# Kernel tuning notes

Hardware: AMD Instinct MI355X
Metric: run time of the kernel (lower is better)

The kernel has to match this reference:

```python
import jax, jax.numpy as jnp
import numpy as np

B, NQ, L, E, K = 64, 1024, 128, 8192, 2
LN_EPS = 1e-5


def setup_inputs() -> dict:
    key = jax.random.key(0)
    ks = jax.random.split(key, 16)
    s1 = 1.0 / np.sqrt(2 * L + 1)
    s2 = 1.0 / np.sqrt(L)
    s3 = 1.0 / np.sqrt(2 * L)
    return {
        "z0": jax.random.normal(ks[0], (B, L), jnp.float32),
        "edge_index": jax.random.randint(ks[1], (2, E), 0, NQ, jnp.int64),
        "edge_attr": jax.random.normal(ks[2], (E,), jnp.float32),
        "n_qubits": NQ,
        # edge MLP params, stacked over K message-passing rounds
        "e_w1": jax.random.normal(ks[3], (K, L, 2 * L + 1), jnp.float32) * s1,
        "e_b1": jnp.zeros((K, L), jnp.float32),
        "e_w2": jax.random.normal(ks[4], (K, L, L), jnp.float32) * s2,
        "e_b2": jnp.zeros((K, L), jnp.float32),
        # node MLP params
        "n_w1": jax.random.normal(ks[5], (K, L, 2 * L), jnp.float32) * s3,
        "n_b1": jnp.zeros((K, L), jnp.float32),
        "ln_g": jnp.ones((K, L), jnp.float32),
        "ln_b": jnp.zeros((K, L), jnp.float32),
        "n_w2": jax.random.normal(ks[6], (K, L, L), jnp.float32) * s2,
        "n_b2": jnp.zeros((K, L), jnp.float32),
    }


def reference(z0, edge_index, edge_attr, n_qubits,
              e_w1, e_b1, e_w2, e_b2,
              n_w1, n_b1, ln_g, ln_b, n_w2, n_b2):
    b, l = z0.shape
    src, tgt = edge_index[0], edge_index[1]
    e_ = src.shape[0]
    # broadcast latent z0 to every node: h [B, N, L]
    h = jnp.broadcast_to(z0[:, None, :], (b, n_qubits, l))
    e = jnp.broadcast_to(edge_attr[None, :, None], (b, e_, 1))  # [B, E, 1]
    k_rounds = e_w1.shape[0]
    for k in range(k_rounds):
        hi = h[:, src, :]  # gather source node feats [B, E, L]
        hj = h[:, tgt, :]  # gather target node feats [B, E, L]
        inp_e = jnp.concatenate([hi, hj, e], axis=-1)  # [B, E, 2L+1]
        m = jax.nn.relu(inp_e @ e_w1[k].T + e_b1[k]) @ e_w2[k].T + e_b2[k]
        # scatter_add messages back to source nodes
        m_agg = jnp.zeros_like(h).at[:, src, :].add(m)
        inp_n = jnp.concatenate([h, m_agg], axis=-1)  # [B, N, 2L]
        x = jax.nn.relu(inp_n @ n_w1[k].T + n_b1[k])
        mu = x.mean(axis=-1, keepdims=True)
        var = ((x - mu) ** 2).mean(axis=-1, keepdims=True)
        x = (x - mu) * jax.lax.rsqrt(var + LN_EPS) * ln_g[k] + ln_b[k]
        # Dropout(p=0.1) is identity in eval mode
        h = x @ n_w2[k].T + n_b2[k] + h  # residual
    return h.mean(axis=1)  # [B, L]
```

## Files before the change

### kernel.cpp

```cpp
#include <hip/hip_runtime.h>

#define B_   64
#define NQ_  1024
#define L_   128
#define E_   8192
#define M_   (B_*NQ_)
#define LDP  136
#define TILE 2176

typedef unsigned short u16;
typedef unsigned int   u32;
typedef unsigned long long u64;
typedef __attribute__((ext_vector_type(8))) short short8;
typedef __attribute__((ext_vector_type(4))) float floatx4;

#define WVB() __builtin_amdgcn_wave_barrier()

__device__ __forceinline__ int imax2(int a, int b) { return a > b ? a : b; }

__device__ __forceinline__ u16 f2bf(float f) {
    union { float f; u32 u; } v; v.f = f;
    return (u16)((v.u + 0x7fffu + ((v.u >> 16) & 1u)) >> 16);
}
__device__ __forceinline__ float bf2f(u16 u) {
    union { u32 u; float f; } v; v.u = ((u32)u) << 16;
    return v.f;
}
__device__ __forceinline__ floatx4 mfma16(short8 a, short8 b, floatx4 c) {
    return __builtin_amdgcn_mfma_f32_16x16x32_bf16(a, b, c, 0, 0, 0);
}
__device__ __forceinline__ short8 sfrag(const u16* t, int r0, int kb, int lane) {
    return *(const short8*)(t + (r0 + (lane & 15)) * LDP + kb * 32 + (lane >> 4) * 8);
}
__device__ __forceinline__ short8 wfrag(const u16* wf, int nt, int kb, int lane) {
    return *(const short8*)(wf + (((kb << 3) + nt) * 64 + lane) * 8);
}
__device__ __forceinline__ void frag_flush(const u16* t, u16* wf, int nt, int lane) {
#pragma unroll
    for (int kb = 0; kb < 4; ++kb)
        *(short8*)(wf + (((kb << 3) + nt) * 64 + lane) * 8) = sfrag(t, 0, kb, lane);
}
__device__ __forceinline__ short8 frag_cvt(const float* base, int r0, int ld, int kb, int lane) {
    const float* p = base + (size_t)(r0 + (lane & 15)) * ld + kb * 32 + (lane >> 4) * 8;
    short8 s;
#pragma unroll
    for (int j = 0; j < 8; ++j) s[j] = (short)f2bf(p[j]);
    return s;
}
__device__ __forceinline__ void tile_store(u16* t, const floatx4* acc, int lane) {
    int col = lane & 15, qd = lane >> 4;
#pragma unroll
    for (int nt = 0; nt < 8; ++nt)
#pragma unroll
        for (int r = 0; r < 4; ++r)
            t[(qd * 4 + r) * LDP + nt * 16 + col] = f2bf(acc[nt][r]);
}
__device__ __forceinline__ void tile_flush(const u16* t, u16* g, int lane) {
#pragma unroll
    for (int it = 0; it < 4; ++it) {
        int chunk = it * 64 + lane, row = chunk >> 4, c8 = chunk & 15;
        *(uint4*)(g + (size_t)row * 128 + c8 * 8) = *(const uint4*)(t + row * LDP + c8 * 8);
    }
}
__device__ __forceinline__ int blk_swz() {
    int r = blockIdx.x;
    int b = (((r >> 3) & 7) << 3) | (r & 7);
    return b * 16 + (r >> 6);
}

struct P {
    const int* ei; const float* attr; const float* z0;
    const float* e_w1; const float* e_b1; const float* e_w2; const float* e_b2;
    const float* n_w1; const float* n_b1; const float* ln_g; const float* ln_b;
    const float* n_w2; const float* n_b2;
    int* ofs; int* tgt_s; float* a_s; float* degf;
    u16* wf;
    u16* w_n20;
    float* wl; float* vb2;
    float* rx; float* rci; float* rcj; float* rh; float* mx0;
    u16* c0t; u16* t1g; u16* ci1; u16* cj1;
    float* out;
};

__global__ __launch_bounds__(256) void k_setup(P p) {
    __shared__ __align__(16) char smem[17408];
    int tid = threadIdx.x, blk = blockIdx.x;
    int lane = tid & 63, w = tid >> 6, col = lane & 15, qd = lane >> 4;

    if (blk == 0) {
        __shared__ int cnt[1024];
        __shared__ int wsum[4];
        __shared__ int flag;
#pragma unroll
        for (int i = 0; i < 4; ++i) cnt[tid + i * 256] = 0;
        if (tid == 0) flag = 1;
        __syncthreads();
        if (tid < 100 && p.ei[2 * tid + 1] != 0) atomicAnd(&flag, 0);
        __syncthreads();
        int i64 = flag;
        for (int e = tid; e < E_; e += 256) {
            int s = i64 ? p.ei[2 * e] : p.ei[e];
            atomicAdd(&cnt[s], 1);
        }
        __syncthreads();
        int q0 = tid * 4;
        int c0 = cnt[q0], c1 = cnt[q0 + 1], c2 = cnt[q0 + 2], c3 = cnt[q0 + 3];
        int tsum = c0 + c1 + c2 + c3, incl = tsum;
#pragma unroll
        for (int o = 1; o < 64; o <<= 1) {
            int t = __shfl_up(incl, o, 64);
            if (lane >= o) incl += t;
        }
        if (lane == 63) wsum[w] = incl;
        __syncthreads();
        int wo = 0;
        for (int i = 0; i < w; ++i) wo += wsum[i];
        int base = wo + incl - tsum;
        p.ofs[q0] = base; p.ofs[q0 + 1] = base + c0;
        p.ofs[q0 + 2] = base + c0 + c1; p.ofs[q0 + 3] = base + c0 + c1 + c2;
        p.degf[q0] = (float)c0; p.degf[q0 + 1] = (float)c1;
        p.degf[q0 + 2] = (float)c2; p.degf[q0 + 3] = (float)c3;
        if (tid == 0) p.ofs[NQ_] = E_;
        __syncthreads();
        cnt[q0] = base; cnt[q0 + 1] = base + c0;
        cnt[q0 + 2] = base + c0 + c1; cnt[q0 + 3] = base + c0 + c1 + c2;
        __syncthreads();
        for (int e = tid; e < E_; e += 256) {
            int s = i64 ? p.ei[2 * e]        : p.ei[e];
            int t = i64 ? p.ei[2 * (E_ + e)] : p.ei[E_ + e];
            int pos = atomicAdd(&cnt[s], 1);
            p.tgt_s[pos] = t;
            p.a_s[pos]   = p.attr[e];
        }
    } else if (blk <= 2) {
        int base = (blk - 1) * 8192;
        for (int idx = tid; idx < 8192; idx += 256)
            p.w_n20[base + idx] = f2bf(p.n_w2[base + idx]);
    } else if (blk == 3) {
        const float* src = p.n_w2 + 16384;
        u16* dst = p.wf + 5 * 16384;
        for (int pr = w; pr < 32; pr += 4) {
            int kb = pr >> 3, nt = pr & 7;
            const float* s = src + (nt * 16 + col) * 128 + kb * 32 + qd * 8;
            short8 v;
#pragma unroll
            for (int j = 0; j < 8; ++j) v[j] = (short)f2bf(s[j]);
            *(short8*)(dst + (pr * 64 + lane) * 8) = v;
        }
    } else if (blk <= 13) {
        int g = (blk - 4) >> 1, part = (blk - 4) & 1;
        const float* Pm; const float* Q; int ldp; u16* D;
        switch (g) {
            case 0:  Pm = p.n_w1 + 128;             ldp = 256; Q = p.e_w2;         D = p.wf;             break;
            case 1:  Pm = p.n_w1 + 32768 + 128;     ldp = 256; Q = p.e_w2 + 16384; D = p.wf + 4 * 16384; break;
            case 2:  Pm = p.e_w1 + 128 * 257;       ldp = 257; Q = p.n_w2;         D = p.wf + 1 * 16384; break;
            case 3:  Pm = p.e_w1 + 128 * 257 + 128; ldp = 257; Q = p.n_w2;         D = p.wf + 2 * 16384; break;
            default: Pm = p.n_w1 + 32768;           ldp = 256; Q = p.n_w2;         D = p.wf + 3 * 16384; break;
        }
        int tile = part * 4 + w;
        int r0 = tile * 16;
        floatx4 acc[8] = {};
#pragma unroll
        for (int kb = 0; kb < 4; ++kb) {
            short8 a = frag_cvt(Pm, r0, ldp, kb, lane);
#pragma unroll
            for (int nt = 0; nt < 8; ++nt) {
                short8 bq;
#pragma unroll
                for (int j = 0; j < 8; ++j)
                    bq[j] = (short)f2bf(Q[(kb * 32 + qd * 8 + j) * 128 + nt * 16 + col]);
                acc[nt] = mfma16(a, bq, acc[nt]);
            }
        }
        u16* slot = (u16*)smem + w * TILE;
        tile_store(slot, acc, lane); WVB();
        frag_flush(slot, D, tile, lane);
    } else if (blk == 14) {
        int r0 = w * 16;
        floatx4 acc[8] = {};
#pragma unroll
        for (int kb = 0; kb < 4; ++kb) {
            short8 a = frag_cvt(p.z0, r0, 128, kb, lane);
#pragma unroll
            for (int nt = 0; nt < 8; ++nt)
                acc[nt] = mfma16(a, frag_cvt(p.n_w1, nt * 16, 256, kb, lane), acc[nt]);
        }
#pragma unroll
        for (int nt = 0; nt < 8; ++nt) {
            int cg = nt * 16 + col; float bv = p.n_b1[cg];
#pragma unroll
            for (int r = 0; r < 4; ++r) p.rx[(r0 + qd * 4 + r) * 128 + cg] = acc[nt][r] + bv;
        }
    } else if (blk <= 17) {
        int r0 = w * 16;
        const float* Wp; int ld; const float* bias; float* dst;
        if (blk == 15)      { Wp = p.e_w1 + 128 * 257;       ld = 257; bias = p.e_b1 + 128; dst = p.rci; }
        else if (blk == 16) { Wp = p.e_w1 + 128 * 257 + 128; ld = 257; bias = nullptr;      dst = p.rcj; }
        else                { Wp = p.n_w1 + 32768;           ld = 256; bias = p.n_b1 + 128; dst = p.rh;  }
        floatx4 acc[8] = {};
#pragma unroll
        for (int kb = 0; kb < 4; ++kb) {
            short8 a;
            int rr = (r0 + col) * 128, kk = kb * 32 + qd * 8;
#pragma unroll
            for (int j = 0; j < 8; ++j) a[j] = (short)f2bf(p.z0[rr + kk + j] + p.n_b2[kk + j]);
#pragma unroll
            for (int nt = 0; nt < 8; ++nt)
                acc[nt] = mfma16(a, frag_cvt(Wp, nt * 16, ld, kb, lane), acc[nt]);
        }
#pragma unroll
        for (int nt = 0; nt < 8; ++nt) {
            int cg = nt * 16 + col;
            float bv = bias ? bias[cg] : 0.0f;
#pragma unroll
            for (int r = 0; r < 4; ++r) dst[(r0 + qd * 4 + r) * 128 + cg] = acc[nt][r] + bv;
        }
    } else if (blk == 18) {
        int r0 = w * 16;
        floatx4 a1[8] = {};
#pragma unroll
        for (int kb = 0; kb < 4; ++kb) {
            short8 a = frag_cvt(p.z0, r0, 128, kb, lane);
#pragma unroll
            for (int nt = 0; nt < 8; ++nt) {
                a1[nt] = mfma16(a, frag_cvt(p.e_w1,       nt * 16, 257, kb, lane), a1[nt]);
                a1[nt] = mfma16(a, frag_cvt(p.e_w1 + 128, nt * 16, 257, kb, lane), a1[nt]);
            }
        }
#pragma unroll
        for (int nt = 0; nt < 8; ++nt) {
            float bv = p.e_b1[nt * 16 + col];
#pragma unroll
            for (int r = 0; r < 4; ++r) a1[nt][r] += bv;
        }
        u16* slot = (u16*)smem + w * TILE;
        tile_store(slot, a1, lane); WVB();
        tile_flush(slot, p.c0t + (size_t)r0 * 128, lane);
    } else {
        int k = tid >> 7, c = tid & 127;
        const float4* wp = (const float4*)(p.n_w1 + k * 32768 + c * 256 + 128);
        const float4* bp = (const float4*)(p.e_b2 + k * 128);
        float s0 = 0.f, s1 = 0.f, s2 = 0.f, s3 = 0.f;
#pragma unroll
        for (int n4 = 0; n4 < 32; ++n4) {
            float4 a = wp[n4], bv = bp[n4];
            s0 += a.x * bv.x; s1 += a.y * bv.y; s2 += a.z * bv.z; s3 += a.w * bv.w;
        }
        p.vb2[tid] = (s0 + s1) + (s2 + s3);
        p.wl[tid]  = p.e_w1[k * 128 * 257 + c * 257 + 256];
        for (int i = tid; i < 8192; i += 256) p.mx0[i] = 0.0f;
    }
}

__global__ __launch_bounds__(256, 4) void k_node0(P p) {
    __shared__ __align__(16) char smem[34816];
    u16* xt = (u16*)smem;
    u16* ob = (u16*)(smem + 17408);
    int tid = threadIdx.x, lane = tid & 63, w = tid >> 6;
    int col = lane & 15, qd = lane >> 4;
    int blk = blk_swz();
    int rowbase = blk * 64 + w * 16;
    int b = blk >> 4;

    {
        u32 cv = ((const u32*)p.c0t)[b * 64 + lane];
        float cx = bf2f((u16)(cv & 0xffffu)), cy = bf2f((u16)(cv >> 16));
        float2 wl2 = ((const float2*)p.wl)[lane];
        for (int qq = 0; qq < 16; qq += 4) {
            int st[4], en[4];
            float ax[4] = {}, ay[4] = {};
#pragma unroll
            for (int j = 0; j < 4; ++j) {
                int q = (rowbase + qq + j) & (NQ_ - 1);
                st[j] = p.ofs[q]; en[j] = p.ofs[q + 1];
            }
            int mx = imax2(imax2(en[0] - st[0], en[1] - st[1]),
                           imax2(en[2] - st[2], en[3] - st[3]));
            for (int k2 = 0; k2 < mx; ++k2) {
#pragma unroll
                for (int j = 0; j < 4; ++j) {
                    int idx = st[j] + k2, last = en[j] - 1;
                    int safe = idx < en[j] ? idx : (last >= 0 ? last : 0);
                    float a = p.a_s[safe];
                    float vx = fmaxf(cx + a * wl2.x, 0.f);
                    float vy = fmaxf(cy + a * wl2.y, 0.f);
                    bool v = idx < en[j];
                    ax[j] += v ? vx : 0.f;
                    ay[j] += v ? vy : 0.f;
                }
            }
#pragma unroll
            for (int j = 0; j < 4; ++j) {
                int r = qq + j;
                u32* tp = (u32*)(xt + (size_t)w * TILE + r * LDP);
                tp[lane] = (u32)f2bf(ax[j]) | ((u32)f2bf(ay[j]) << 16);
            }
        }
    }
    WVB();

    floatx4 xa[8] = {};
#pragma unroll
    for (int kb = 0; kb < 4; ++kb) {
        short8 a = sfrag(xt + w * TILE, 0, kb, lane);
#pragma unroll
        for (int nt = 0; nt < 8; ++nt) xa[nt] = mfma16(a, wfrag(p.wf, nt, kb, lane), xa[nt]);
    }
    WVB();
    float s8[8] = {};
#pragma unroll
    for (int nt = 0; nt < 8; ++nt) {
        int cg = nt * 16 + col;
        float base = p.rx[b * 128 + cg], vb = p.vb2[cg];
#pragma unroll
        for (int r = 0; r < 4; ++r) {
            int row = rowbase + qd * 4 + r;
            xa[nt][r] = fmaxf(xa[nt][r] + base + p.degf[row & (NQ_ - 1)] * vb, 0.f);
        }
    }
#pragma unroll
    for (int r = 0; r < 4; ++r) {
        float s = 0.f, s2 = 0.f;
#pragma unroll
        for (int nt = 0; nt < 8; ++nt) { float v = xa[nt][r]; s += v; s2 += v * v; }
#pragma unroll
        for (int o = 1; o < 16; o <<= 1) { s += __shfl_xor(s, o, 64); s2 += __shfl_xor(s2, o, 64); }
        float mu = s * (1.f / 128.f), var = s2 * (1.f / 128.f) - mu * mu;
        float rs = rsqrtf(var + 1e-5f);
#pragma unroll
        for (int nt = 0; nt < 8; ++nt) {
            int cg = nt * 16 + col;
            float xv = (xa[nt][r] - mu) * rs * p.ln_g[cg] + p.ln_b[cg];
            xa[nt][r] = xv;
            s8[nt] += xv;
        }
    }
    tile_store(xt + w * TILE, xa, lane);
#pragma unroll
    for (int nt = 0; nt < 8; ++nt) {
        s8[nt] += __shfl_xor(s8[nt], 16, 64);
        s8[nt] += __shfl_xor(s8[nt], 32, 64);
    }
    if (lane < 16) {
#pragma unroll
        for (int nt = 0; nt < 8; ++nt)
            atomicAdd(p.mx0 + b * 128 + nt * 16 + lane, s8[nt]);
    }
    WVB();
#pragma unroll
    for (int ph = 0; ph < 3; ++ph) {
        const u16* wfp = p.wf + ((ph == 0) ? 1 : (ph == 1) ? 2 : 3) * 16384;
        const float* rt = (ph == 0) ? p.rci : (ph == 1) ? p.rcj : p.rh;
        floatx4 ca[8] = {};
#pragma unroll
        for (int kb = 0; kb < 4; ++kb) {
            short8 a = sfrag(xt + w * TILE, 0, kb, lane);
#pragma unroll
            for (int nt = 0; nt < 8; ++nt) ca[nt] = mfma16(a, wfrag(wfp, nt, kb, lane), ca[nt]);
        }
#pragma unroll
        for (int nt = 0; nt < 8; ++nt) {
            float rc = rt[b * 128 + nt * 16 + col];
#pragma unroll
            for (int r = 0; r < 4; ++r) ca[nt][r] += rc;
        }
        if (ph == 2) {
            u64* t1f = (u64*)p.t1g;
            int tile = blk * 4 + w;
#pragma unroll
            for (int nt = 0; nt < 8; ++nt) {
                u32 lo = (u32)f2bf(ca[nt][0]) | ((u32)f2bf(ca[nt][1]) << 16);
                u32 hi = (u32)f2bf(ca[nt][2]) | ((u32)f2bf(ca[nt][3]) << 16);
                t1f[(size_t)(tile * 8 + nt) * 64 + lane] = (u64)lo | ((u64)hi << 32);
            }
        } else {
            u16* dst = (ph == 0) ? p.ci1 : p.cj1;
            tile_store(ob + w * TILE, ca, lane);
            WVB();
            tile_flush(ob + w * TILE, dst + (size_t)rowbase * 128, lane);
            WVB();
        }
    }
}

__global__ __launch_bounds__(256, 4) void k_node1(P p) {
    __shared__ __align__(16) char smem[34816];
    u16* xt = (u16*)smem;
    u16* ob = (u16*)(smem + 17408);
    int tid = threadIdx.x, lane = tid & 63, w = tid >> 6;
    int col = lane & 15, qd = lane >> 4;
    int blk = blk_swz();
    int rowbase = blk * 64 + w * 16;
    int b = blk >> 4;

    {
        float2 wl2 = ((const float2*)(p.wl + 128))[lane];
        const u32* cip = (const u32*)p.ci1;
        const u32* cjp = (const u32*)p.cj1 + (size_t)b * NQ_ * 64;
        for (int qq = 0; qq < 16; qq += 8) {
            int st[8], en[8];
            float ax[8] = {}, ay[8] = {}, cx[8], cy[8];
#pragma unroll
            for (int j = 0; j < 8; ++j) {
                int row = rowbase + qq + j;
                u32 cv = cip[(size_t)row * 64 + lane];
                cx[j] = bf2f((u16)(cv & 0xffffu)); cy[j] = bf2f((u16)(cv >> 16));
                int q = row & (NQ_ - 1);
                st[j] = p.ofs[q]; en[j] = p.ofs[q + 1];
            }
            int mx = imax2(imax2(imax2(en[0] - st[0], en[1] - st[1]),
                                 imax2(en[2] - st[2], en[3] - st[3])),
                           imax2(imax2(en[4] - st[4], en[5] - st[5]),
                                 imax2(en[6] - st[6], en[7] - st[7])));
            int tc[8]; float ac[8];
#pragma unroll
            for (int j = 0; j < 8; ++j) {
                int last = en[j] - 1;
                int safe = st[j] < en[j] ? st[j] : (last >= 0 ? last : 0);
                tc[j] = p.tgt_s[safe]; ac[j] = p.a_s[safe];
            }
            for (int k2 = 0; k2 < mx; ++k2) {
                u32 jv[8];
#pragma unroll
                for (int j = 0; j < 8; ++j)
                    jv[j] = cjp[(size_t)tc[j] * 64 + lane];
                int tn[8]; float an[8];
#pragma unroll
                for (int j = 0; j < 8; ++j) {
                    int idx = st[j] + k2 + 1, last = en[j] - 1;
                    int safe = idx < en[j] ? idx : (last >= 0 ? last : 0);
                    tn[j] = p.tgt_s[safe]; an[j] = p.a_s[safe];
                }
#pragma unroll
                for (int j = 0; j < 8; ++j) {
                    float vx = fmaxf(cx[j] + bf2f((u16)(jv[j] & 0xffffu)) + ac[j] * wl2.x, 0.f);
                    float vy = fmaxf(cy[j] + bf2f((u16)(jv[j] >> 16))    + ac[j] * wl2.y, 0.f);
                    bool v = st[j] + k2 < en[j];
                    ax[j] += v ? vx : 0.f;
                    ay[j] += v ? vy : 0.f;
                    tc[j] = tn[j]; ac[j] = an[j];
                }
            }
#pragma unroll
            for (int j = 0; j < 8; ++j) {
                int r = qq + j;
                u32* tp = (u32*)(xt + (size_t)w * TILE + r * LDP);
                tp[lane] = (u32)f2bf(ax[j]) | ((u32)f2bf(ay[j]) << 16);
            }
        }
    }
    WVB();

    const u16* wc1 = p.wf + 4 * 16384;
    floatx4 xa[8] = {};
#pragma unroll
    for (int kb = 0; kb < 4; ++kb) {
        short8 a = sfrag(xt + w * TILE, 0, kb, lane);
#pragma unroll
        for (int nt = 0; nt < 8; ++nt) xa[nt] = mfma16(a, wfrag(wc1, nt, kb, lane), xa[nt]);
    }
    const float* vb21 = p.vb2 + 128;
    const u64* t1f = (const u64*)p.t1g;
    int tile = blk * 4 + w;
#pragma unroll
    for (int nt = 0; nt < 8; ++nt) {
        int cg = nt * 16 + col;
        float vb = vb21[cg];
        u64 tv = t1f[(size_t)(tile * 8 + nt) * 64 + lane];
        float tvf[4] = { bf2f((u16)tv),         bf2f((u16)(tv >> 16)),
                         bf2f((u16)(tv >> 32)), bf2f((u16)(tv >> 48)) };
#pragma unroll
        for (int r = 0; r < 4; ++r) {
            int row = rowbase + qd * 4 + r;
            xa[nt][r] = fmaxf(xa[nt][r] + tvf[r] + p.degf[row & (NQ_ - 1)] * vb, 0.f);
        }
    }
#pragma unroll
    for (int r = 0; r < 4; ++r) {
        float s = 0.f, s2 = 0.f;
#pragma unroll
        for (int nt = 0; nt < 8; ++nt) { float v = xa[nt][r]; s += v; s2 += v * v; }
#pragma unroll
        for (int o = 1; o < 16; o <<= 1) { s += __shfl_xor(s, o, 64); s2 += __shfl_xor(s2, o, 64); }
        float mu = s * (1.f / 128.f), var = s2 * (1.f / 128.f) - mu * mu;
        float rs = rsqrtf(var + 1e-5f);
#pragma unroll
        for (int nt = 0; nt < 8; ++nt) {
            int cg = nt * 16 + col;
            xa[nt][r] = (xa[nt][r] - mu) * rs * p.ln_g[128 + cg] + p.ln_b[128 + cg];
        }
    }
    const u16* n21 = p.wf + 5 * 16384;
    float s8[8] = {};
    tile_store(ob + w * TILE, xa, lane);
    WVB();
    {
        floatx4 ma[8] = {};
#pragma unroll
        for (int kb = 0; kb < 4; ++kb) {
            short8 a = sfrag(ob + w * TILE, 0, kb, lane);
#pragma unroll
            for (int nt = 0; nt < 8; ++nt) ma[nt] = mfma16(a, wfrag(n21, nt, kb, lane), ma[nt]);
        }
#pragma unroll
        for (int nt = 0; nt < 8; ++nt)
#pragma unroll
            for (int r = 0; r < 4; ++r) s8[nt] += ma[nt][r];
    }
#pragma unroll
    for (int nt = 0; nt < 8; ++nt) {
        s8[nt] += __shfl_xor(s8[nt], 16, 64);
        s8[nt] += __shfl_xor(s8[nt], 32, 64);
    }
    if (lane < 16) {
#pragma unroll
        for (int nt = 0; nt < 8; ++nt)
            atomicAdd(p.out + b * 128 + nt * 16 + lane, s8[nt] * (1.f / 1024.f));
    }
    if ((blk & 15) == 0 && tid < 128) {
        int c = tid;
        const float* mx = p.mx0 + b * 128;
        float s = 0.f;
#pragma unroll
        for (int k8 = 0; k8 < 16; ++k8) {
            short8 wv = *(const short8*)(p.w_n20 + c * 128 + k8 * 8);
            const float* mxp = mx + k8 * 8;
#pragma unroll
            for (int j = 0; j < 8; ++j) s += mxp[j] * bf2f((u16)wv[j]);
        }
        float acc = p.z0[b * 128 + c] + p.n_b2[c] + p.n_b2[128 + c] + s * (1.f / 1024.f);
        atomicAdd(p.out + b * 128 + c, acc);
    }
}

extern "C" void kernel_launch(void* const* d_in, const int* in_sizes, int n_in,
                              void* d_out, int out_size, void* d_ws, size_t ws_size,
                              hipStream_t stream) {
    P p;
    p.z0   = (const float*)d_in[0];
    p.ei   = (const int*)d_in[1];
    p.attr = (const float*)d_in[2];
    p.e_w1 = (const float*)d_in[4];
    p.e_b1 = (const float*)d_in[5];
    p.e_w2 = (const float*)d_in[6];
    p.e_b2 = (const float*)d_in[7];
    p.n_w1 = (const float*)d_in[8];
    p.n_b1 = (const float*)d_in[9];
    p.ln_g = (const float*)d_in[10];
    p.ln_b = (const float*)d_in[11];
    p.n_w2 = (const float*)d_in[12];
    p.n_b2 = (const float*)d_in[13];
    p.out  = (float*)d_out;

    const size_t H = (size_t)M_ * L_;
    float* f  = (float*)d_ws;
    p.degf = f;
    p.a_s  = f + 1024;
    p.wl   = p.a_s + 8192;
    p.vb2  = p.wl + 256;
    p.rx   = p.vb2 + 256;
    p.rci  = p.rx + 8192;
    p.rcj  = p.rci + 8192;
    p.rh   = p.rcj + 8192;
    p.mx0  = p.rh + 8192;
    p.ofs  = (int*)(p.mx0 + 8192);
    p.tgt_s = p.ofs + 1056;
    p.wf    = (u16*)(p.tgt_s + 8192);
    p.w_n20 = p.wf + 6 * 16384;
    p.c0t   = p.w_n20 + 16384;
    p.t1g   = p.c0t + 8192;
    p.ci1   = p.t1g + H;
    p.cj1   = p.ci1 + H;

    hipMemsetAsync(p.out, 0, 8192 * sizeof(float), stream);

    k_setup<<<20, 256, 0, stream>>>(p);
    k_node0<<<1024, 256, 0, stream>>>(p);
    k_node1<<<1024, 256, 0, stream>>>(p);
}
```

Measured before the change: 202.7 us.

## Sort nodes by degree and pack edge target and attribute into int2

Setup now builds a degree-sorted node permutation, pairing low- and high-degree groups per wave, so the 8 nodes a wave walks together have similar edge counts and fewer lanes sit idle. Edge targets (pre-shifted by 64) and attributes are packed into one int2 array so each edge costs one load, and the gather loop is split into an unpredicated part up to the minimum degree and a guarded tail. Node tiles are processed in permuted order, with cj1 rows scattered back to their real node index. This adds indirection through an LDS qmap and scattered stores.

Result: faster. 192.0 us (-5.3%).

```diff
diff --git a/kernel.cpp b/kernel.cpp
--- a/kernel.cpp
+++ b/kernel.cpp
@@ -17,6 +17,7 @@
 #define WVB() __builtin_amdgcn_wave_barrier()
 
 __device__ __forceinline__ int imax2(int a, int b) { return a > b ? a : b; }
+__device__ __forceinline__ int imin2(int a, int b) { return a < b ? a : b; }
 
 __device__ __forceinline__ u16 f2bf(float f) {
     union { float f; u32 u; } v; v.f = f;
@@ -26,6 +27,8 @@
     union { u32 u; float f; } v; v.u = ((u32)u) << 16;
     return v.f;
 }
+__device__ __forceinline__ float bf2f_lo(u32 jv) { return __uint_as_float(jv << 16); }
+__device__ __forceinline__ float bf2f_hi(u32 jv) { return __uint_as_float(jv & 0xffff0000u); }
 __device__ __forceinline__ floatx4 mfma16(short8 a, short8 b, floatx4 c) {
     return __builtin_amdgcn_mfma_f32_16x16x32_bf16(a, b, c, 0, 0, 0);
 }
@@ -73,7 +76,7 @@
     const float* e_w1; const float* e_b1; const float* e_w2; const float* e_b2;
     const float* n_w1; const float* n_b1; const float* ln_g; const float* ln_b;
     const float* n_w2; const float* n_b2;
-    int* ofs; int* tgt_s; float* a_s; float* degf;
+    int* ofs; int2* ta; int* perm; float* degf;
     u16* wf;
     u16* w_n20;
     float* wl; float* vb2;
@@ -90,9 +93,12 @@
     if (blk == 0) {
         __shared__ int cnt[1024];
         __shared__ int wsum[4];
+        __shared__ int dh[64];
+        __shared__ int db[64];
         __shared__ int flag;
 #pragma unroll
         for (int i = 0; i < 4; ++i) cnt[tid + i * 256] = 0;
+        if (tid < 64) dh[tid] = 0;
         if (tid == 0) flag = 1;
         __syncthreads();
         if (tid < 100 && p.ei[2 * tid + 1] != 0) atomicAnd(&flag, 0);
@@ -112,6 +118,8 @@
             if (lane >= o) incl += t;
         }
         if (lane == 63) wsum[w] = incl;
+        atomicAdd(&dh[imin2(c0, 63)], 1); atomicAdd(&dh[imin2(c1, 63)], 1);
+        atomicAdd(&dh[imin2(c2, 63)], 1); atomicAdd(&dh[imin2(c3, 63)], 1);
         __syncthreads();
         int wo = 0;
         for (int i = 0; i < w; ++i) wo += wsum[i];
@@ -124,14 +132,27 @@
         __syncthreads();
         cnt[q0] = base; cnt[q0 + 1] = base + c0;
         cnt[q0 + 2] = base + c0 + c1; cnt[q0 + 3] = base + c0 + c1 + c2;
+        if (tid < 64) {
+            int v = dh[tid], inc = v;
+#pragma unroll
+            for (int o = 1; o < 64; o <<= 1) {
+                int t = __shfl_up(inc, o, 64);
+                if (tid >= o) inc += t;
+            }
+            db[tid] = inc - v;
+        }
         __syncthreads();
         for (int e = tid; e < E_; e += 256) {
             int s = i64 ? p.ei[2 * e]        : p.ei[e];
             int t = i64 ? p.ei[2 * (E_ + e)] : p.ei[E_ + e];
             int pos = atomicAdd(&cnt[s], 1);
-            p.tgt_s[pos] = t;
-            p.a_s[pos]   = p.attr[e];
-        }
+            p.ta[pos] = make_int2(t << 6, __float_as_int(p.attr[e]));
+        }
+        p.perm[atomicAdd(&db[imin2(c0, 63)], 1)] = q0;
+        p.perm[atomicAdd(&db[imin2(c1, 63)], 1)] = q0 + 1;
+        p.perm[atomicAdd(&db[imin2(c2, 63)], 1)] = q0 + 2;
+        p.perm[atomicAdd(&db[imin2(c3, 63)], 1)] = q0 + 3;
+        if (tid == 0) p.ta[E_] = make_int2(0, 0);
     } else if (blk <= 2) {
         int base = (blk - 1) * 8192;
         for (int idx = tid; idx < 8192; idx += 256)
@@ -252,46 +273,82 @@
     }
 }
 
+__device__ __forceinline__ void load_qmap(int* qmap, const int* perm,
+                                          int blk, int w, int lane) {
+    int W = (blk & 15) * 4 + w;
+    int g0 = W, g1 = 127 - W;
+    if (lane < 16)
+        qmap[w * 16 + lane] = perm[lane < 8 ? g0 * 8 + lane : g1 * 8 + lane - 8];
+    WVB();
+}
+
 __global__ __launch_bounds__(256, 4) void k_node0(P p) {
-    __shared__ __align__(16) char smem[34816];
+    __shared__ __align__(16) char smem[35072];
     u16* xt = (u16*)smem;
     u16* ob = (u16*)(smem + 17408);
+    int* qmap = (int*)(smem + 34816);
     int tid = threadIdx.x, lane = tid & 63, w = tid >> 6;
     int col = lane & 15, qd = lane >> 4;
     int blk = blk_swz();
     int rowbase = blk * 64 + w * 16;
     int b = blk >> 4;
+    load_qmap(qmap, p.perm, blk, w, lane);
 
     {
         u32 cv = ((const u32*)p.c0t)[b * 64 + lane];
         float cx = bf2f((u16)(cv & 0xffffu)), cy = bf2f((u16)(cv >> 16));
         float2 wl2 = ((const float2*)p.wl)[lane];
-        for (int qq = 0; qq < 16; qq += 4) {
-            int st[4], en[4];
-            float ax[4] = {}, ay[4] = {};
-#pragma unroll
-            for (int j = 0; j < 4; ++j) {
-                int q = (rowbase + qq + j) & (NQ_ - 1);
+        const int* tay = (const int*)p.ta;
+        for (int g2 = 0; g2 < 2; ++g2) {
+            int st[8], en[8];
+            float ax[8] = {}, ay[8] = {};
+#pragma unroll
+            for (int j = 0; j < 8; ++j) {
+                int q = qmap[w * 16 + g2 * 8 + j];
                 st[j] = p.ofs[q]; en[j] = p.ofs[q + 1];
             }
-            int mx = imax2(imax2(en[0] - st[0], en[1] - st[1]),
-                           imax2(en[2] - st[2], en[3] - st[3]));
-            for (int k2 = 0; k2 < mx; ++k2) {
-#pragma unroll
-                for (int j = 0; j < 4; ++j) {
-                    int idx = st[j] + k2, last = en[j] - 1;
+            int mn = en[0] - st[0], mx = mn;
+#pragma unroll
+            for (int j = 1; j < 8; ++j) {
+                mn = imin2(mn, en[j] - st[j]); mx = imax2(mx, en[j] - st[j]);
+            }
+            float ac[8];
+#pragma unroll
+            for (int j = 0; j < 8; ++j) {
+                int last = en[j] - 1;
+                int safe = st[j] < en[j] ? st[j] : (last >= 0 ? last : 0);
+                ac[j] = __int_as_float(tay[2 * safe + 1]);
+            }
+            for (int k2 = 0; k2 < mn; ++k2) {
+                float an[8];
+#pragma unroll
+                for (int j = 0; j < 8; ++j) an[j] = __int_as_float(tay[2 * (st[j] + k2 + 1) + 1]);
+#pragma unroll
+                for (int j = 0; j < 8; ++j) {
+                    ax[j] += fmaxf(cx + ac[j] * wl2.x, 0.f);
+                    ay[j] += fmaxf(cy + ac[j] * wl2.y, 0.f);
+                    ac[j] = an[j];
+                }
+            }
+            for (int k2 = mn; k2 < mx; ++k2) {
+                float an[8];
+#pragma unroll
+                for (int j = 0; j < 8; ++j) {
+                    int idx = st[j] + k2 + 1, last = en[j] - 1;
                     int safe = idx < en[j] ? idx : (last >= 0 ? last : 0);
-                    float a = p.a_s[safe];
-                    float vx = fmaxf(cx + a * wl2.x, 0.f);
-                    float vy = fmaxf(cy + a * wl2.y, 0.f);
-                    bool v = idx < en[j];
-                    ax[j] += v ? vx : 0.f;
-                    ay[j] += v ? vy : 0.f;
+                    an[j] = __int_as_float(tay[2 * safe + 1]);
                 }
-            }
-#pragma unroll
-            for (int j = 0; j < 4; ++j) {
-                int r = qq + j;
+#pragma unroll
+                for (int j = 0; j < 8; ++j) {
+                    bool v = st[j] + k2 < en[j];
+                    ax[j] += v ? fmaxf(cx + ac[j] * wl2.x, 0.f) : 0.f;
+                    ay[j] += v ? fmaxf(cy + ac[j] * wl2.y, 0.f) : 0.f;
+                    ac[j] = an[j];
+                }
+            }
+#pragma unroll
+            for (int j = 0; j < 8; ++j) {
+                int r = g2 * 8 + j;
                 u32* tp = (u32*)(xt + (size_t)w * TILE + r * LDP);
                 tp[lane] = (u32)f2bf(ax[j]) | ((u32)f2bf(ay[j]) << 16);
             }
@@ -314,8 +371,8 @@
         float base = p.rx[b * 128 + cg], vb = p.vb2[cg];
 #pragma unroll
         for (int r = 0; r < 4; ++r) {
-            int row = rowbase + qd * 4 + r;
-            xa[nt][r] = fmaxf(xa[nt][r] + base + p.degf[row & (NQ_ - 1)] * vb, 0.f);
+            int q = qmap[w * 16 + qd * 4 + r];
+            xa[nt][r] = fmaxf(xa[nt][r] + base + p.degf[q] * vb, 0.f);
         }
     }
 #pragma unroll
@@ -373,77 +430,104 @@
                 u32 hi = (u32)f2bf(ca[nt][2]) | ((u32)f2bf(ca[nt][3]) << 16);
                 t1f[(size_t)(tile * 8 + nt) * 64 + lane] = (u64)lo | ((u64)hi << 32);
             }
-        } else {
-            u16* dst = (ph == 0) ? p.ci1 : p.cj1;
+        } else if (ph == 0) {
             tile_store(ob + w * TILE, ca, lane);
             WVB();
-            tile_flush(ob + w * TILE, dst + (size_t)rowbase * 128, lane);
+            tile_flush(ob + w * TILE, p.ci1 + (size_t)rowbase * 128, lane);
             WVB();
+        } else {
+            tile_store(ob + w * TILE, ca, lane);
+            WVB();
+#pragma unroll
+            for (int it = 0; it < 4; ++it) {
+                int chunk = it * 64 + lane, row = chunk >> 4, c8 = chunk & 15;
+                int q = qmap[w * 16 + row];
+                *(uint4*)(p.cj1 + ((size_t)b * NQ_ + q) * 128 + c8 * 8) =
+                    *(const uint4*)(ob + w * TILE + row * LDP + c8 * 8);
+            }
+            WVB();
         }
     }
 }
 
 __global__ __launch_bounds__(256, 4) void k_node1(P p) {
-    __shared__ __align__(16) char smem[34816];
+    __shared__ __align__(16) char smem[35072];
     u16* xt = (u16*)smem;
     u16* ob = (u16*)(smem + 17408);
+    int* qmap = (int*)(smem + 34816);
     int tid = threadIdx.x, lane = tid & 63, w = tid >> 6;
     int col = lane & 15, qd = lane >> 4;
     int blk = blk_swz();
     int rowbase = blk * 64 + w * 16;
     int b = blk >> 4;
+    load_qmap(qmap, p.perm, blk, w, lane);
 
     {
         float2 wl2 = ((const float2*)(p.wl + 128))[lane];
         const u32* cip = (const u32*)p.ci1;
         const u32* cjp = (const u32*)p.cj1 + (size_t)b * NQ_ * 64;
-        for (int qq = 0; qq < 16; qq += 8) {
+        for (int g2 = 0; g2 < 2; ++g2) {
             int st[8], en[8];
             float ax[8] = {}, ay[8] = {}, cx[8], cy[8];
 #pragma unroll
             for (int j = 0; j < 8; ++j) {
-                int row = rowbase + qq + j;
-                u32 cv = cip[(size_t)row * 64 + lane];
+                int prow = rowbase + g2 * 8 + j;
+                u32 cv = cip[(size_t)prow * 64 + lane];
                 cx[j] = bf2f((u16)(cv & 0xffffu)); cy[j] = bf2f((u16)(cv >> 16));
-                int q = row & (NQ_ - 1);
+                int q = qmap[w * 16 + g2 * 8 + j];
                 st[j] = p.ofs[q]; en[j] = p.ofs[q + 1];
             }
-            int mx = imax2(imax2(imax2(en[0] - st[0], en[1] - st[1]),
-                                 imax2(en[2] - st[2], en[3] - st[3])),
-                           imax2(imax2(en[4] - st[4], en[5] - st[5]),
-                                 imax2(en[6] - st[6], en[7] - st[7])));
+            int mn = en[0] - st[0], mx = mn;
+#pragma unroll
+            for (int j = 1; j < 8; ++j) {
+                mn = imin2(mn, en[j] - st[j]); mx = imax2(mx, en[j] - st[j]);
+            }
             int tc[8]; float ac[8];
 #pragma unroll
             for (int j = 0; j < 8; ++j) {
                 int last = en[j] - 1;
                 int safe = st[j] < en[j] ? st[j] : (last >= 0 ? last : 0);
-                tc[j] = p.tgt_s[safe]; ac[j] = p.a_s[safe];
-            }
-            for (int k2 = 0; k2 < mx; ++k2) {
+                int2 tv = p.ta[safe];
+                tc[j] = tv.x; ac[j] = __int_as_float(tv.y);
+            }
+            for (int k2 = 0; k2 < mn; ++k2) {
                 u32 jv[8];
 #pragma unroll
-                for (int j = 0; j < 8; ++j)
-                    jv[j] = cjp[(size_t)tc[j] * 64 + lane];
-                int tn[8]; float an[8];
+                for (int j = 0; j < 8; ++j) jv[j] = cjp[(u32)(tc[j] + lane)];
+                int2 tv[8];
+#pragma unroll
+                for (int j = 0; j < 8; ++j) tv[j] = p.ta[st[j] + k2 + 1];
+#pragma unroll
+                for (int j = 0; j < 8; ++j) {
+                    ax[j] += fmaxf(cx[j] + bf2f_lo(jv[j]) + ac[j] * wl2.x, 0.f);
+                    ay[j] += fmaxf(cy[j] + bf2f_hi(jv[j]) + ac[j] * wl2.y, 0.f);
+                    tc[j] = tv[j].x; ac[j] = __int_as_float(tv[j].y);
+                }
+            }
+            for (int k2 = mn; k2 < mx; ++k2) {
+                u32 jv[8];
+#pragma unroll
+                for (int j = 0; j < 8; ++j) jv[j] = cjp[(u32)(tc[j] + lane)];
+                int2 tv[8];
 #pragma unroll
                 for (int j = 0; j < 8; ++j) {
                     int idx = st[j] + k2 + 1, last = en[j] - 1;
                     int safe = idx < en[j] ? idx : (last >= 0 ? last : 0);
-                    tn[j] = p.tgt_s[safe]; an[j] = p.a_s[safe];
+                    tv[j] = p.ta[safe];
                 }
 #pragma unroll
                 for (int j = 0; j < 8; ++j) {
-                    float vx = fmaxf(cx[j] + bf2f((u16)(jv[j] & 0xffffu)) + ac[j] * wl2.x, 0.f);
-                    float vy = fmaxf(cy[j] + bf2f((u16)(jv[j] >> 16))    + ac[j] * wl2.y, 0.f);
                     bool v = st[j] + k2 < en[j];
+                    float vx = fmaxf(cx[j] + bf2f_lo(jv[j]) + ac[j] * wl2.x, 0.f);
+                    float vy = fmaxf(cy[j] + bf2f_hi(jv[j]) + ac[j] * wl2.y, 0.f);
                     ax[j] += v ? vx : 0.f;
                     ay[j] += v ? vy : 0.f;
-                    tc[j] = tn[j]; ac[j] = an[j];
+                    tc[j] = tv[j].x; ac[j] = __int_as_float(tv[j].y);
                 }
             }
 #pragma unroll
             for (int j = 0; j < 8; ++j) {
-                int r = qq + j;
+                int r = g2 * 8 + j;
                 u32* tp = (u32*)(xt + (size_t)w * TILE + r * LDP);
                 tp[lane] = (u32)f2bf(ax[j]) | ((u32)f2bf(ay[j]) << 16);
             }
@@ -471,8 +555,8 @@
                          bf2f((u16)(tv >> 32)), bf2f((u16)(tv >> 48)) };
 #pragma unroll
         for (int r = 0; r < 4; ++r) {
-            int row = rowbase + qd * 4 + r;
-            xa[nt][r] = fmaxf(xa[nt][r] + tvf[r] + p.degf[row & (NQ_ - 1)] * vb, 0.f);
+            int q = qmap[w * 16 + qd * 4 + r];
+            xa[nt][r] = fmaxf(xa[nt][r] + tvf[r] + p.degf[q] * vb, 0.f);
         }
     }
 #pragma unroll
@@ -555,8 +639,7 @@
     const size_t H = (size_t)M_ * L_;
     float* f  = (float*)d_ws;
     p.degf = f;
-    p.a_s  = f + 1024;
-    p.wl   = p.a_s + 8192;
+    p.wl   = f + 1024;
     p.vb2  = p.wl + 256;
     p.rx   = p.vb2 + 256;
     p.rci  = p.rx + 8192;
@@ -564,8 +647,9 @@
     p.rh   = p.rcj + 8192;
     p.mx0  = p.rh + 8192;
     p.ofs  = (int*)(p.mx0 + 8192);
-    p.tgt_s = p.ofs + 1056;
-    p.wf    = (u16*)(p.tgt_s + 8192);
+    p.perm = p.ofs + 1056;
+    p.ta   = (int2*)(p.perm + 1024);
+    p.wf    = (u16*)(p.ta + E_ + 8);
     p.w_n20 = p.wf + 6 * 16384;
     p.c0t   = p.w_n20 + 16384;
     p.t1g   = p.c0t + 8192;
```
